# Kernel optimization log

Measured on AMD Instinct MI355X. Metric: run time of the kernel, lower is better.

## Reference

```python
import jax, jax.numpy as jnp
import numpy as np

DIM = 1024
D_STATE = 64
D_CONV = 4
EXPAND = 2
HEADDIM = 64
D_INNER = EXPAND * DIM                      # 2048
NHEADS = D_INNER // HEADDIM                 # 32
D_CONV_DIM = D_INNER + 2 * D_STATE          # 2176 (ngroups=1)
D_IN_PROJ = 2 * D_INNER + 2 * D_STATE + NHEADS  # 4256


def setup_inputs() -> dict:
    key = jax.random.key(0)
    ks = jax.random.split(key, 9)
    B, L = 4, 2048
    x = jax.random.normal(ks[0], (B, L, DIM), dtype=jnp.float32)
    in_proj_w = jax.random.normal(ks[1], (D_IN_PROJ, DIM), dtype=jnp.float32) * 0.02
    conv_w = jax.random.normal(ks[2], (D_CONV_DIM, D_CONV), dtype=jnp.float32) * 0.2
    conv_b = jax.random.normal(ks[3], (D_CONV_DIM,), dtype=jnp.float32) * 0.02
    # dt bias from inverse-softplus of dt ~ U(1e-3, 0.1) (mamba2 init)
    dt = jnp.exp(jax.random.uniform(ks[4], (NHEADS,)) * (np.log(0.1) - np.log(1e-3)) + np.log(1e-3))
    dt_bias = (dt + jnp.log(-jnp.expm1(-dt))).astype(jnp.float32)
    A_log = jnp.log(jax.random.uniform(ks[5], (NHEADS,), minval=1.0, maxval=16.0)).astype(jnp.float32)
    D = jnp.ones((NHEADS,), dtype=jnp.float32)
    norm_w = jnp.ones((D_INNER,), dtype=jnp.float32)
    out_proj_w = jax.random.normal(ks[6], (DIM, D_INNER), dtype=jnp.float32) * 0.02
    return {"x": x, "in_proj_w": in_proj_w, "conv_w": conv_w, "conv_b": conv_b,
            "dt_bias": dt_bias, "A_log": A_log, "D": D, "norm_w": norm_w,
            "out_proj_w": out_proj_w}


def _mamba2_fwd(x, in_proj_w, conv_w, conv_b, dt_bias, A_log, D, norm_w, out_proj_w):
    B, L, _ = x.shape
    zxbcdt = jnp.einsum('bld,ed->ble', x, in_proj_w)  # (B,L,4256)
    z = zxbcdt[..., :D_INNER]
    xBC = zxbcdt[..., D_INNER:D_INNER + D_CONV_DIM]
    dt = jax.nn.softplus(zxbcdt[..., D_INNER + D_CONV_DIM:] + dt_bias)  # (B,L,H)
    # causal depthwise conv (kernel D_CONV) + silu
    xp = jnp.pad(xBC, ((0, 0), (D_CONV - 1, 0), (0, 0)))
    conv = conv_b
    for k in range(D_CONV):
        conv = conv + xp[:, k:k + L, :] * conv_w[:, k]
    xBC = jax.nn.silu(conv)
    x_ssm = xBC[..., :D_INNER].reshape(B, L, NHEADS, HEADDIM)
    Bm = xBC[..., D_INNER:D_INNER + D_STATE]          # (B,L,N) ngroups=1
    Cm = xBC[..., D_INNER + D_STATE:]                 # (B,L,N)
    A = -jnp.exp(A_log)                               # (H,)

    def step(h, inp):
        xt, Bt, Ct, dtt = inp                         # (B,H,P),(B,N),(B,N),(B,H)
        dA = jnp.exp(dtt * A)                         # (B,H)
        h = h * dA[:, :, None, None] + (dtt[:, :, None] * xt)[..., None] * Bt[:, None, None, :]
        y = jnp.einsum('bhpn,bn->bhp', h, Ct)
        return h, y

    h0 = jnp.zeros((B, NHEADS, HEADDIM, D_STATE), dtype=x.dtype)
    xs = (jnp.swapaxes(x_ssm, 0, 1), jnp.swapaxes(Bm, 0, 1),
          jnp.swapaxes(Cm, 0, 1), jnp.swapaxes(dt, 0, 1))
    _, ys = jax.lax.scan(step, h0, xs)                # (L,B,H,P)
    y = jnp.swapaxes(ys, 0, 1) + x_ssm * D[None, None, :, None]
    y = y.reshape(B, L, D_INNER)
    # gated RMSNorm (norm_before_gate=False): norm(y * silu(z))
    g = y * jax.nn.silu(z)
    g = g * jax.lax.rsqrt(jnp.mean(g * g, axis=-1, keepdims=True) + 1e-5) * norm_w
    return jnp.einsum('ble,de->bld', g, out_proj_w)


def reference(x, in_proj_w, conv_w, conv_b, dt_bias, A_log, D, norm_w, out_proj_w):
    return _mamba2_fwd(x, in_proj_w, conv_w, conv_b, dt_bias, A_log, D, norm_w, out_proj_w)
```

## Files before the change

### kernel.cpp

```cpp
#include <hip/hip_runtime.h>
#include <stdint.h>

typedef unsigned short ushort_t;
typedef __attribute__((ext_vector_type(4))) float f32x4;
typedef __attribute__((ext_vector_type(8))) short short8;
typedef __attribute__((ext_vector_type(4))) unsigned short us4;

#define L_SEQ   2048
#define NROWS   8192
#define KDIM    1024
#define DINNER  2048
#define NHEADS  32
#define DSTATE  64
#define DCONVD  2176
#define NPROJ   4256
#define NPROJP  4352
#define LDZX    4352
#define NCHUNK  32

__device__ __forceinline__ float bf2f(ushort_t u) {
    union { uint32_t i; float f; } v; v.i = ((uint32_t)u) << 16; return v.f;
}
__device__ __forceinline__ ushort_t f2bf(float f) {
    uint32_t x = __float_as_uint(f);
    x += 0x7FFFu + ((x >> 16) & 1u);
    return (ushort_t)(x >> 16);
}
__device__ __forceinline__ int swzi(int row, int col) {
    return row * 64 + (col ^ ((row & 7) << 3));
}

__global__ __launch_bounds__(256) void cast_bf16_kernel(const float* __restrict__ in,
                                                        ushort_t* __restrict__ out, int n4) {
    int i = blockIdx.x * 256 + threadIdx.x;
    if (i >= n4) return;
    float4 v = ((const float4*)in)[i];
    ushort4 o;
    o.x = f2bf(v.x); o.y = f2bf(v.y); o.z = f2bf(v.z); o.w = f2bf(v.w);
    ((ushort4*)out)[i] = o;
}

__global__ __launch_bounds__(256) void cast_pad_w_kernel(const float* __restrict__ w,
                                                         ushort_t* __restrict__ out) {
    int i = blockIdx.x * 256 + threadIdx.x;
    int idx = i * 4;
    int row = idx >> 10;
    ushort4 o;
    if (row < NPROJ) {
        float4 v = ((const float4*)w)[i];
        o.x = f2bf(v.x); o.y = f2bf(v.y); o.z = f2bf(v.z); o.w = f2bf(v.w);
    } else {
        o.x = 0; o.y = 0; o.z = 0; o.w = 0;
    }
    ((ushort4*)out)[i] = o;
}

__device__ __forceinline__ void async16(const void* g, void* l) {
    __builtin_amdgcn_global_load_lds((const __attribute__((address_space(1))) void*)g,
                                     (__attribute__((address_space(3))) void*)l, 16, 0, 0);
}

template<bool OUT_BF16>
__global__ __launch_bounds__(256) void gemm_bt_kernel(const ushort_t* __restrict__ A,
                                                      const ushort_t* __restrict__ B,
                                                      void* __restrict__ Cp,
                                                      const int K, const int ldc) {
    __shared__ ushort_t As[4096];
    __shared__ ushort_t Bs[4096];
    const int tid  = threadIdx.x;
    const int wave = tid >> 6;
    const int lane = tid & 63;
    const int llo  = lane & 15;
    const int lhi  = lane >> 4;
    const int m0 = blockIdx.y * 128;
    const int n0 = blockIdx.x * 128;
    const int wr = wave >> 1, wc = wave & 1;

    f32x4 acc[4][4];
    const f32x4 zero = {0.f, 0.f, 0.f, 0.f};
#pragma unroll
    for (int i = 0; i < 4; ++i)
#pragma unroll
        for (int j = 0; j < 4; ++j) acc[i][j] = zero;

    const int srow = tid >> 2;
    const int skq  = tid & 3;
    const ushort_t* gA = A + (size_t)(m0 + srow) * K + skq * 8;
    const ushort_t* gB = B + (size_t)(n0 + srow) * K + skq * 8;
    ushort_t* lA0 = As + wave * 512;
    ushort_t* lA1 = As + 2048 + wave * 512;
    ushort_t* lB0 = Bs + wave * 512;
    ushort_t* lB1 = Bs + 2048 + wave * 512;
    const size_t rstep = (size_t)64 * K;

    const ushort_t* pa = As + (wr * 64 + llo) * 32 + lhi * 8;
    const ushort_t* pb = Bs + (wc * 64 + llo) * 32 + lhi * 8;

    for (int k0 = 0; k0 < K; k0 += 32) {
        __syncthreads();
        async16(gA + k0, lA0);
        async16(gA + rstep + k0, lA1);
        async16(gB + k0, lB0);
        async16(gB + rstep + k0, lB1);
        __syncthreads();
        short8 af[4], bfr[4];
#pragma unroll
        for (int i = 0; i < 4; ++i) af[i]  = *(const short8*)(pa + i * 512);
#pragma unroll
        for (int j = 0; j < 4; ++j) bfr[j] = *(const short8*)(pb + j * 512);
#pragma unroll
        for (int i = 0; i < 4; ++i)
#pragma unroll
            for (int j = 0; j < 4; ++j)
                acc[i][j] = __builtin_amdgcn_mfma_f32_16x16x32_bf16(af[i], bfr[j], acc[i][j], 0, 0, 0);
    }

#pragma unroll
    for (int i = 0; i < 4; ++i)
#pragma unroll
        for (int j = 0; j < 4; ++j) {
            const int col = n0 + wc * 64 + j * 16 + llo;
            const int rowb = m0 + wr * 64 + i * 16 + lhi * 4;
#pragma unroll
            for (int r = 0; r < 4; ++r) {
                if (OUT_BF16) {
                    ((ushort_t*)Cp)[(size_t)(rowb + r) * ldc + col] = f2bf(acc[i][j][r]);
                } else {
                    ((float*)Cp)[(size_t)(rowb + r) * ldc + col] = acc[i][j][r];
                }
            }
        }
}

__global__ __launch_bounds__(256) void conv_silu_kernel(const ushort_t* __restrict__ zx,
                                                        const float* __restrict__ conv_w,
                                                        const float* __restrict__ conv_b,
                                                        ushort_t* __restrict__ convout) {
    const int c = blockIdx.x * 256 + threadIdx.x;
    const int row = blockIdx.y;
    if (c >= DCONVD) return;
    const int l = row & (L_SEQ - 1);
    float acc = conv_b[c];
#pragma unroll
    for (int k = 0; k < 4; ++k) {
        int ll = l - 3 + k;
        if (ll >= 0)
            acc += bf2f(zx[(size_t)(row - 3 + k) * LDZX + DINNER + c]) * conv_w[c * 4 + k];
    }
    float s = acc / (1.f + expf(-acc));
    convout[(size_t)row * DCONVD + c] = f2bf(s);
}

__global__ __launch_bounds__(256) void dt_kernel(const ushort_t* __restrict__ zx,
                                                 const float* __restrict__ dt_bias,
                                                 float* __restrict__ dtb) {
    int idx = blockIdx.x * 256 + threadIdx.x;
    int row = idx >> 5;
    int h = idx & 31;
    float v = bf2f(zx[(size_t)row * LDZX + NPROJ - NHEADS + h]) + dt_bias[h];
    dtb[idx] = (v > 20.f) ? v : log1pf(expf(v));
}

__global__ __launch_bounds__(256) void chunk_intra_kernel(
    const ushort_t* __restrict__ cvb, const float* __restrict__ dtb,
    const float* __restrict__ A_log, const float* __restrict__ Dvec,
    ushort_t* __restrict__ ybuf, ushort_t* __restrict__ Gbuf,
    float* __restrict__ expPb)
{
    const int c = blockIdx.x, h = blockIdx.y, b = blockIdx.z;
    const int tid = threadIdx.x;
    const int wv = tid >> 6, lane = tid & 63;
    const int lr = lane & 15, lk = lane >> 4;

    __shared__ __align__(16) ushort_t Cs[4096];
    __shared__ __align__(16) ushort_t Bs[4096];
    __shared__ __align__(16) ushort_t Xt[4096];
    __shared__ __align__(16) ushort_t Ss[4096];
    __shared__ __align__(16) ushort_t Bw[4096];
    __shared__ float sP[64], sdt[64], sWf[64];

    const int t4 = tid >> 2, qq = tid & 3;
    const size_t rowg0 = (size_t)b * L_SEQ + c * 64;
    const ushort_t* rowp = cvb + (rowg0 + t4) * DCONVD;

    short8 rb0 = *(const short8*)(rowp + DINNER + qq * 16);
    short8 rb1 = *(const short8*)(rowp + DINNER + qq * 16 + 8);
    short8 rc0 = *(const short8*)(rowp + DINNER + DSTATE + qq * 16);
    short8 rc1 = *(const short8*)(rowp + DINNER + DSTATE + qq * 16 + 8);
    short8 rx0 = *(const short8*)(rowp + h * 64 + qq * 16);
    short8 rx1 = *(const short8*)(rowp + h * 64 + qq * 16 + 8);

    *(short8*)&Cs[swzi(t4, qq * 16)]     = rc0;
    *(short8*)&Cs[swzi(t4, qq * 16 + 8)] = rc1;
    *(short8*)&Bs[swzi(t4, qq * 16)]     = rb0;
    *(short8*)&Bs[swzi(t4, qq * 16 + 8)] = rb1;
#pragma unroll
    for (int k = 0; k < 8; ++k) {
        Xt[swzi(qq * 16 + k, t4)]     = (ushort_t)rx0[k];
        Xt[swzi(qq * 16 + 8 + k, t4)] = (ushort_t)rx1[k];
    }
    if (tid < 64) {
        float dt = dtb[(rowg0 + tid) * NHEADS + h];
        float A = -__expf(A_log[h]);
        float P = dt * A;
#pragma unroll
        for (int off = 1; off < 64; off <<= 1) {
            float o = __shfl_up(P, off);
            if (tid >= off) P += o;
        }
        sP[tid] = P;
        sdt[tid] = dt;
        float P63 = __shfl(P, 63);
        sWf[tid] = __expf(P63 - P) * dt;
        expPb[(size_t)(b * NHEADS + h) * L_SEQ + c * 64 + tid] = __expf(P);
    }
    __syncthreads();

    {
        const float w = sWf[t4];
#pragma unroll
        for (int k = 0; k < 8; ++k) {
            Bw[swzi(qq * 16 + k, t4)]     = f2bf(bf2f((ushort_t)rb0[k]) * w);
            Bw[swzi(qq * 16 + 8 + k, t4)] = f2bf(bf2f((ushort_t)rb1[k]) * w);
        }
    }

    const float Dh = Dvec[h];
    {
        short8 a0 = *(const short8*)&Cs[swzi(wv * 16 + lr, lk * 8)];
        short8 a1 = *(const short8*)&Cs[swzi(wv * 16 + lr, 32 + lk * 8)];
        f32x4 acc[4];
        const f32x4 zero = {0.f, 0.f, 0.f, 0.f};
#pragma unroll
        for (int nj = 0; nj < 4; ++nj) {
            short8 b0 = *(const short8*)&Bs[swzi(nj * 16 + lr, lk * 8)];
            short8 b1 = *(const short8*)&Bs[swzi(nj * 16 + lr, 32 + lk * 8)];
            acc[nj] = __builtin_amdgcn_mfma_f32_16x16x32_bf16(a0, b0, zero, 0, 0, 0);
            acc[nj] = __builtin_amdgcn_mfma_f32_16x16x32_bf16(a1, b1, acc[nj], 0, 0, 0);
        }
#pragma unroll
        for (int r = 0; r < 4; ++r) {
            const int i = wv * 16 + lk * 4 + r;
            const float Pi = sP[i];
#pragma unroll
            for (int nj = 0; nj < 4; ++nj) {
                const int j = nj * 16 + lr;
                float s = 0.f;
                if (j <= i) s = acc[nj][r] * __expf(Pi - sP[j]) * sdt[j];
                if (j == i) s += Dh;
                Ss[swzi(i, j)] = f2bf(s);
            }
        }
    }
    __syncthreads();

    {
        short8 a0 = *(const short8*)&Ss[swzi(wv * 16 + lr, lk * 8)];
        short8 a1 = *(const short8*)&Ss[swzi(wv * 16 + lr, 32 + lk * 8)];
        const f32x4 zero = {0.f, 0.f, 0.f, 0.f};
#pragma unroll
        for (int np = 0; np < 4; ++np) {
            short8 b0 = *(const short8*)&Xt[swzi(np * 16 + lr, lk * 8)];
            short8 b1 = *(const short8*)&Xt[swzi(np * 16 + lr, 32 + lk * 8)];
            f32x4 acc = __builtin_amdgcn_mfma_f32_16x16x32_bf16(a0, b0, zero, 0, 0, 0);
            acc = __builtin_amdgcn_mfma_f32_16x16x32_bf16(a1, b1, acc, 0, 0, 0);
#pragma unroll
            for (int r = 0; r < 4; ++r) {
                const int i = wv * 16 + lk * 4 + r;
                const int p = np * 16 + lr;
                ybuf[(rowg0 + i) * DINNER + (size_t)h * 64 + p] = f2bf(acc[r]);
            }
        }
    }

    {
        short8 a0 = *(const short8*)&Xt[swzi(wv * 16 + lr, lk * 8)];
        short8 a1 = *(const short8*)&Xt[swzi(wv * 16 + lr, 32 + lk * 8)];
        const f32x4 zero = {0.f, 0.f, 0.f, 0.f};
        const size_t gbase = ((size_t)((b * NHEADS + h) * NCHUNK + c)) << 12;
#pragma unroll
        for (int nt = 0; nt < 4; ++nt) {
            short8 b0 = *(const short8*)&Bw[swzi(nt * 16 + lr, lk * 8)];
            short8 b1 = *(const short8*)&Bw[swzi(nt * 16 + lr, 32 + lk * 8)];
            f32x4 acc = __builtin_amdgcn_mfma_f32_16x16x32_bf16(a0, b0, zero, 0, 0, 0);
            acc = __builtin_amdgcn_mfma_f32_16x16x32_bf16(a1, b1, acc, 0, 0, 0);
#pragma unroll
            for (int r = 0; r < 4; ++r) {
                const int p = wv * 16 + lk * 4 + r;
                const int n = nt * 16 + lr;
                Gbuf[gbase + p * 64 + n] = f2bf(acc[r]);
            }
        }
    }
}

__global__ __launch_bounds__(256) void state_scan_kernel(
    ushort_t* __restrict__ GH, const float* __restrict__ expPb)
{
    const int half = blockIdx.x, h = blockIdx.y, b = blockIdx.z;
    const int bh = b * NHEADS + h;
    const int e0 = half * 2048 + threadIdx.x * 8;
    ushort_t* base = GH + ((size_t)bh << 17);
    const float* ep = expPb + (size_t)bh * L_SEQ;

    float hr[8];
#pragma unroll
    for (int k = 0; k < 8; ++k) hr[k] = 0.f;

    short8 g = *(const short8*)(base + e0);
    float Ec = ep[63];
    for (int c = 0; c < NCHUNK; ++c) {
        short8 gn = g; float En = 0.f;
        if (c + 1 < NCHUNK) {
            gn = *(const short8*)(base + ((size_t)(c + 1) << 12) + e0);
            En = ep[(c + 1) * 64 + 63];
        }
        short8 o;
#pragma unroll
        for (int k = 0; k < 8; ++k) o[k] = (short)f2bf(hr[k]);
        *(short8*)(base + ((size_t)c << 12) + e0) = o;
#pragma unroll
        for (int k = 0; k < 8; ++k) hr[k] = hr[k] * Ec + bf2f((ushort_t)g[k]);
        g = gn; Ec = En;
    }
}

__global__ __launch_bounds__(256) void y_inter_kernel(
    const ushort_t* __restrict__ cvb, const float* __restrict__ expPb,
    const ushort_t* __restrict__ hst, ushort_t* __restrict__ ybuf)
{
    const int c = blockIdx.x + 1, h = blockIdx.y, b = blockIdx.z;
    const int tid = threadIdx.x;
    const int wv = tid >> 6, lane = tid & 63;
    const int lr = lane & 15, lk = lane >> 4;
    const int bh = b * NHEADS + h;

    __shared__ __align__(16) ushort_t Cs[4096];
    __shared__ __align__(16) ushort_t Hp[4096];
    __shared__ float sEp[64];

    const int t4 = tid >> 2, qq = tid & 3;
    const size_t rowg0 = (size_t)b * L_SEQ + c * 64;
    {
        const ushort_t* rp = cvb + (rowg0 + t4) * DCONVD + DINNER + DSTATE + qq * 16;
        *(short8*)&Cs[swzi(t4, qq * 16)]     = *(const short8*)rp;
        *(short8*)&Cs[swzi(t4, qq * 16 + 8)] = *(const short8*)(rp + 8);
        const ushort_t* hr = hst + (((size_t)(bh * NCHUNK + c)) << 12) + t4 * 64 + qq * 16;
        *(short8*)&Hp[swzi(t4, qq * 16)]     = *(const short8*)hr;
        *(short8*)&Hp[swzi(t4, qq * 16 + 8)] = *(const short8*)(hr + 8);
    }
    if (tid < 64) sEp[tid] = expPb[(size_t)bh * L_SEQ + c * 64 + tid];
    __syncthreads();

    short8 a0 = *(const short8*)&Cs[swzi(wv * 16 + lr, lk * 8)];
    short8 a1 = *(const short8*)&Cs[swzi(wv * 16 + lr, 32 + lk * 8)];
    const f32x4 zero = {0.f, 0.f, 0.f, 0.f};
#pragma unroll
    for (int np = 0; np < 4; ++np) {
        short8 b0 = *(const short8*)&Hp[swzi(np * 16 + lr, lk * 8)];
        short8 b1 = *(const short8*)&Hp[swzi(np * 16 + lr, 32 + lk * 8)];
        f32x4 acc = __builtin_amdgcn_mfma_f32_16x16x32_bf16(a0, b0, zero, 0, 0, 0);
        acc = __builtin_amdgcn_mfma_f32_16x16x32_bf16(a1, b1, acc, 0, 0, 0);
#pragma unroll
        for (int r = 0; r < 4; ++r) {
            const int t = wv * 16 + lk * 4 + r;
            const int p = np * 16 + lr;
            ushort_t* yp = &ybuf[(rowg0 + t) * DINNER + (size_t)h * 64 + p];
            *yp = f2bf(bf2f(*yp) + acc[r] * sEp[t]);
        }
    }
}

__global__ __launch_bounds__(256) void gatenorm_kernel(const ushort_t* __restrict__ ybuf,
                                                       const ushort_t* __restrict__ zx,
                                                       const float* __restrict__ norm_w,
                                                       ushort_t* __restrict__ gbuf) {
    const int row = blockIdx.x;
    const int tid = threadIdx.x;
    short8 yv = *(const short8*)(ybuf + (size_t)row * DINNER + tid * 8);
    short8 zv = *(const short8*)(zx + (size_t)row * LDZX + tid * 8);
    float g[8];
    float ss = 0.f;
#pragma unroll
    for (int i = 0; i < 8; ++i) {
        float y = bf2f((ushort_t)yv[i]);
        float z = bf2f((ushort_t)zv[i]);
        float sz = z / (1.f + expf(-z));
        float gg = y * sz;
        g[i] = gg;
        ss += gg * gg;
    }
#pragma unroll
    for (int o = 32; o > 0; o >>= 1) ss += __shfl_xor(ss, o);
    __shared__ float wsum[4];
    if ((tid & 63) == 0) wsum[tid >> 6] = ss;
    __syncthreads();
    float tot = wsum[0] + wsum[1] + wsum[2] + wsum[3];
    float scale = rsqrtf(tot * (1.0f / (float)DINNER) + 1e-5f);
    short8 o8;
#pragma unroll
    for (int i = 0; i < 8; ++i)
        o8[i] = (short)f2bf(g[i] * scale * norm_w[tid * 8 + i]);
    *(short8*)(gbuf + (size_t)row * DINNER + tid * 8) = o8;
}

extern "C" void kernel_launch(void* const* d_in, const int* in_sizes, int n_in,
                              void* d_out, int out_size, void* d_ws, size_t ws_size,
                              hipStream_t stream) {
    const float* x          = (const float*)d_in[0];
    const float* in_proj_w  = (const float*)d_in[1];
    const float* conv_w     = (const float*)d_in[2];
    const float* conv_b     = (const float*)d_in[3];
    const float* dt_bias    = (const float*)d_in[4];
    const float* A_log      = (const float*)d_in[5];
    const float* Dvec       = (const float*)d_in[6];
    const float* norm_w     = (const float*)d_in[7];
    const float* out_proj_w = (const float*)d_in[8];
    float* out = (float*)d_out;

    char* ws = (char*)d_ws;
    size_t off = 0;
    ushort_t* owbf  = (ushort_t*)(ws + off); off += (size_t)KDIM * DINNER * 2;
    ushort_t* zx    = (ushort_t*)(ws + off); off += (size_t)NROWS * LDZX * 2;
    ushort_t* cvb   = (ushort_t*)(ws + off); off += (size_t)NROWS * DCONVD * 2;
    float*    dtb   = (float*)(ws + off);    off += (size_t)NROWS * NHEADS * 4;
    float*    expPb = (float*)(ws + off);    off += (size_t)128 * L_SEQ * 4;
    ushort_t* ybuf  = (ushort_t*)(ws + off); off += (size_t)NROWS * DINNER * 2;
    char* tail = ws + off;
    ushort_t* xbf  = (ushort_t*)tail;
    ushort_t* wbf  = (ushort_t*)(tail + (size_t)NROWS * KDIM * 2);
    ushort_t* Gbuf = (ushort_t*)tail;
    ushort_t* gbuf = (ushort_t*)tail;

    cast_bf16_kernel<<<8192, 256, 0, stream>>>(x, xbf, NROWS * KDIM / 4);
    cast_pad_w_kernel<<<4352, 256, 0, stream>>>(in_proj_w, wbf);
    cast_bf16_kernel<<<2048, 256, 0, stream>>>(out_proj_w, owbf, KDIM * DINNER / 4);

    gemm_bt_kernel<true><<<dim3(NPROJP / 128, NROWS / 128), 256, 0, stream>>>(
        xbf, wbf, zx, KDIM, LDZX);

    conv_silu_kernel<<<dim3((DCONVD + 255) / 256, NROWS), 256, 0, stream>>>(zx, conv_w, conv_b, cvb);

    dt_kernel<<<NROWS * NHEADS / 256, 256, 0, stream>>>(zx, dt_bias, dtb);

    chunk_intra_kernel<<<dim3(NCHUNK, NHEADS, 4), 256, 0, stream>>>(
        cvb, dtb, A_log, Dvec, ybuf, Gbuf, expPb);
    state_scan_kernel<<<dim3(2, NHEADS, 4), 256, 0, stream>>>(Gbuf, expPb);
    y_inter_kernel<<<dim3(NCHUNK - 1, NHEADS, 4), 256, 0, stream>>>(
        cvb, expPb, Gbuf, ybuf);

    gatenorm_kernel<<<NROWS, 256, 0, stream>>>(ybuf, zx, norm_w, gbuf);

    gemm_bt_kernel<false><<<dim3(KDIM / 128, NROWS / 128), 256, 0, stream>>>(
        gbuf, owbf, out, DINNER, KDIM);
}
```

Baseline: 345.5 us.

## Replace in_proj GEMM with 256x256-tile double-buffered MFMA kernel

Adds a dedicated in-projection GEMM that uses 256x256 output tiles, 512 threads, XOR-swizzled LDS, and double-buffered async global-to-LDS loads interleaved with MFMA quarters. It also remaps block indices so neighbouring blocks share operand tiles in cache. The aim is more data reuse per LDS load and better overlap of loads with compute than the 128x128 kernel gives. In exchange, occupancy is one block per CU and the 544-block grid is small, which can cause tail imbalance.

```diff
diff --git a/kernel.cpp b/kernel.cpp
--- a/kernel.cpp
+++ b/kernel.cpp
@@ -58,6 +58,110 @@
 __device__ __forceinline__ void async16(const void* g, void* l) {
     __builtin_amdgcn_global_load_lds((const __attribute__((address_space(1))) void*)g,
                                      (__attribute__((address_space(3))) void*)l, 16, 0, 0);
+}
+
+__global__ __launch_bounds__(512, 1) void gemm256_kernel(const ushort_t* __restrict__ A,
+                                                         const ushort_t* __restrict__ B,
+                                                         ushort_t* __restrict__ C) {
+    __shared__ ushort_t lds[2][2][2][8192];
+    const int tid = threadIdx.x;
+    const int w = tid >> 6, l = tid & 63;
+    const int lr = l & 15, lk = l >> 4;
+    const int wm = w >> 2, wn = w & 3;
+
+    const int lin = blockIdx.x;
+    const int swz = (lin & 7) * 68 + (lin >> 3);
+    const int nt = swz % 17, mt = swz / 17;
+    const int m0 = mt * 256, n0 = nt * 256;
+
+    const int row0 = tid >> 3,          c0 = (tid & 7) ^ (row0 & 7);
+    const int row1 = (512 + tid) >> 3,  c1 = ((512 + tid) & 7) ^ (row1 & 7);
+
+    f32x4 acc[8][4];
+    const f32x4 zero = {0.f, 0.f, 0.f, 0.f};
+#pragma unroll
+    for (int i = 0; i < 8; ++i)
+#pragma unroll
+        for (int j = 0; j < 4; ++j) acc[i][j] = zero;
+
+#define STAGE256(d_, mat_, h_, ktn_) do {                                              \
+        const ushort_t* gb_ = ((mat_) == 0 ? A + (size_t)(m0 + (h_) * 128) * KDIM      \
+                                           : B + (size_t)(n0 + (h_) * 128) * KDIM)     \
+                              + (ktn_) * 64;                                           \
+        async16(gb_ + (size_t)row0 * KDIM + c0 * 8, &lds[d_][mat_][h_][w * 512]);      \
+        async16(gb_ + (size_t)row1 * KDIM + c1 * 8, &lds[d_][mat_][h_][4096 + w * 512]);\
+    } while (0)
+
+    STAGE256(0, 0, 0, 0);
+    STAGE256(0, 1, 0, 0);
+    STAGE256(0, 0, 1, 0);
+    STAGE256(0, 1, 1, 0);
+
+    const int NKT = KDIM / 64;
+    for (int kt = 0; kt < NKT; ++kt) {
+        const int d = kt & 1;
+        const ushort_t* Ah = &lds[d][0][wm][0];
+        const ushort_t* Bh = &lds[d][1][wn >> 1][0];
+        const int bcol0 = (wn & 1) * 64;
+#pragma unroll
+        for (int q = 0; q < 4; ++q) {
+            const int qm = q >> 1, qn = q & 1;
+            if (kt + 1 < NKT) {
+                STAGE256(d ^ 1, (q & 1), (q >> 1), kt + 1);
+            }
+            if (q == 0) {
+                if (kt + 1 < NKT) asm volatile("s_waitcnt vmcnt(2)" ::: "memory");
+                else              asm volatile("s_waitcnt vmcnt(0)" ::: "memory");
+            }
+            __builtin_amdgcn_s_barrier();
+            asm volatile("" ::: "memory");
+            short8 af[4][2], bfv[2][2];
+#pragma unroll
+            for (int fr = 0; fr < 4; ++fr) {
+                const int ar = qm * 64 + fr * 16 + lr;
+                const int x7 = ar & 7;
+#pragma unroll
+                for (int ks = 0; ks < 2; ++ks) {
+                    const int k16 = ks * 4 + lk;
+                    af[fr][ks] = *(const short8*)&Ah[ar * 64 + ((k16 ^ x7) << 3)];
+                }
+            }
+#pragma unroll
+            for (int fc = 0; fc < 2; ++fc) {
+                const int br = bcol0 + qn * 32 + fc * 16 + lr;
+                const int x7 = br & 7;
+#pragma unroll
+                for (int ks = 0; ks < 2; ++ks) {
+                    const int k16 = ks * 4 + lk;
+                    bfv[fc][ks] = *(const short8*)&Bh[br * 64 + ((k16 ^ x7) << 3)];
+                }
+            }
+            __builtin_amdgcn_s_setprio(1);
+#pragma unroll
+            for (int ks = 0; ks < 2; ++ks)
+#pragma unroll
+                for (int fr = 0; fr < 4; ++fr)
+#pragma unroll
+                    for (int fc = 0; fc < 2; ++fc)
+                        acc[qm * 4 + fr][qn * 2 + fc] = __builtin_amdgcn_mfma_f32_16x16x32_bf16(
+                            af[fr][ks], bfv[fc][ks], acc[qm * 4 + fr][qn * 2 + fc], 0, 0, 0);
+            __builtin_amdgcn_s_setprio(0);
+            asm volatile("" ::: "memory");
+            __builtin_amdgcn_s_barrier();
+        }
+    }
+
+#pragma unroll
+    for (int fr2 = 0; fr2 < 8; ++fr2)
+#pragma unroll
+        for (int fc2 = 0; fc2 < 4; ++fc2) {
+            const int col = n0 + wn * 64 + fc2 * 16 + lr;
+            const int rowb = m0 + wm * 128 + fr2 * 16 + lk * 4;
+#pragma unroll
+            for (int r = 0; r < 4; ++r)
+                C[(size_t)(rowb + r) * LDZX + col] = f2bf(acc[fr2][fc2][r]);
+        }
+#undef STAGE256
 }
 
 template<bool OUT_BF16>
@@ -436,8 +540,7 @@
     cast_pad_w_kernel<<<4352, 256, 0, stream>>>(in_proj_w, wbf);
     cast_bf16_kernel<<<2048, 256, 0, stream>>>(out_proj_w, owbf, KDIM * DINNER / 4);
 
-    gemm_bt_kernel<true><<<dim3(NPROJP / 128, NROWS / 128), 256, 0, stream>>>(
-        xbf, wbf, zx, KDIM, LDZX);
+    gemm256_kernel<<<544, 512, 0, stream>>>(xbf, wbf, zx);
 
     conv_silu_kernel<<<dim3((DCONVD + 255) / 256, NROWS), 256, 0, stream>>>(zx, conv_w, conv_b, cvb);
 
```

Result: no change. 340.9 us (-1.3%).

## Replace GEMMs with 256-row double-buffered swizzled-LDS tiles; vectorize conv

Applied to the files above, without the earlier changes.

Both projection GEMMs move to a new 512-thread kernel with 256xBN tiles, a K-step of 64, double-buffered async global-to-LDS loads, XOR-swizzled LDS layout to avoid bank conflicts, grid swizzling for L2 locality, and setprio around the MFMA block. This aims to raise data reuse and overlap loads with compute, compared with the old 128x128 single-buffered loop that synchronised twice per step. The conv+silu kernel now handles 8 channels per thread with vector loads and stores. The larger tiles mean fewer blocks (544 and 256), which risks lower occupancy and poor wave balance on the GPU.

```diff
diff --git a/kernel.cpp b/kernel.cpp
--- a/kernel.cpp
+++ b/kernel.cpp
@@ -60,74 +60,109 @@
                                      (__attribute__((address_space(3))) void*)l, 16, 0, 0);
 }
 
-template<bool OUT_BF16>
-__global__ __launch_bounds__(256) void gemm_bt_kernel(const ushort_t* __restrict__ A,
-                                                      const ushort_t* __restrict__ B,
-                                                      void* __restrict__ Cp,
-                                                      const int K, const int ldc) {
-    __shared__ ushort_t As[4096];
-    __shared__ ushort_t Bs[4096];
-    const int tid  = threadIdx.x;
-    const int wave = tid >> 6;
-    const int lane = tid & 63;
-    const int llo  = lane & 15;
-    const int lhi  = lane >> 4;
-    const int m0 = blockIdx.y * 128;
-    const int n0 = blockIdx.x * 128;
-    const int wr = wave >> 1, wc = wave & 1;
-
-    f32x4 acc[4][4];
+template<int BN, bool OUT_BF16>
+__global__ __launch_bounds__(512, 1) void gemm256_kernel(const ushort_t* __restrict__ Ap,
+                                                         const ushort_t* __restrict__ Bp,
+                                                         void* __restrict__ Cp,
+                                                         const int K, const int ldc,
+                                                         const int ntn) {
+    constexpr int NBH = BN / 128;
+    constexpr int FC  = BN / 64;
+    __shared__ ushort_t ldsA[2][2][8192];
+    __shared__ ushort_t ldsB[2][NBH][8192];
+
+    const int tid = threadIdx.x;
+    const int w = tid >> 6, l = tid & 63;
+    const int lr = l & 15, lk = l >> 4;
+    const int wm = w >> 2, wn = w & 3;
+
+    const int lin = blockIdx.x;
+    const int cpx = gridDim.x >> 3;
+    const int swz = (lin & 7) * cpx + (lin >> 3);
+    const int nt = swz % ntn, mt = swz / ntn;
+    const int m0 = mt * 256, n0 = nt * BN;
+
+    const int row0 = tid >> 3,          c0 = (tid & 7) ^ (row0 & 7);
+    const int row1 = (512 + tid) >> 3,  c1 = ((512 + tid) & 7) ^ (row1 & 7);
+
+    const int bcol = wn * (BN / 4);
+    const int bh = bcol >> 7, bw0 = bcol & 127;
+
+    f32x4 acc[8][FC];
     const f32x4 zero = {0.f, 0.f, 0.f, 0.f};
 #pragma unroll
-    for (int i = 0; i < 4; ++i)
-#pragma unroll
-        for (int j = 0; j < 4; ++j) acc[i][j] = zero;
-
-    const int srow = tid >> 2;
-    const int skq  = tid & 3;
-    const ushort_t* gA = A + (size_t)(m0 + srow) * K + skq * 8;
-    const ushort_t* gB = B + (size_t)(n0 + srow) * K + skq * 8;
-    ushort_t* lA0 = As + wave * 512;
-    ushort_t* lA1 = As + 2048 + wave * 512;
-    ushort_t* lB0 = Bs + wave * 512;
-    ushort_t* lB1 = Bs + 2048 + wave * 512;
-    const size_t rstep = (size_t)64 * K;
-
-    const ushort_t* pa = As + (wr * 64 + llo) * 32 + lhi * 8;
-    const ushort_t* pb = Bs + (wc * 64 + llo) * 32 + lhi * 8;
-
-    for (int k0 = 0; k0 < K; k0 += 32) {
-        __syncthreads();
-        async16(gA + k0, lA0);
-        async16(gA + rstep + k0, lA1);
-        async16(gB + k0, lB0);
-        async16(gB + rstep + k0, lB1);
-        __syncthreads();
-        short8 af[4], bfr[4];
-#pragma unroll
-        for (int i = 0; i < 4; ++i) af[i]  = *(const short8*)(pa + i * 512);
-#pragma unroll
-        for (int j = 0; j < 4; ++j) bfr[j] = *(const short8*)(pb + j * 512);
-#pragma unroll
-        for (int i = 0; i < 4; ++i)
-#pragma unroll
-            for (int j = 0; j < 4; ++j)
-                acc[i][j] = __builtin_amdgcn_mfma_f32_16x16x32_bf16(af[i], bfr[j], acc[i][j], 0, 0, 0);
-    }
-
-#pragma unroll
-    for (int i = 0; i < 4; ++i)
-#pragma unroll
-        for (int j = 0; j < 4; ++j) {
-            const int col = n0 + wc * 64 + j * 16 + llo;
-            const int rowb = m0 + wr * 64 + i * 16 + lhi * 4;
+    for (int i = 0; i < 8; ++i)
+#pragma unroll
+        for (int j = 0; j < FC; ++j) acc[i][j] = zero;
+
+    auto stage = [&](int d_, int isB, int h_, int ktn) {
+        const ushort_t* gb = (isB ? Bp + (size_t)(n0 + h_ * 128) * K
+                                  : Ap + (size_t)(m0 + h_ * 128) * K) + (size_t)ktn * 64;
+        ushort_t* lb = isB ? &ldsB[d_][h_][0] : &ldsA[d_][h_][0];
+        async16(gb + (size_t)row0 * K + c0 * 8, lb + w * 512);
+        async16(gb + (size_t)row1 * K + c1 * 8, lb + 4096 + w * 512);
+    };
+
+#define COMPUTE_KS(ks_) do {                                                          \
+        short8 af[8], bfv[FC];                                                        \
+        _Pragma("unroll")                                                             \
+        for (int fr = 0; fr < 8; ++fr) {                                              \
+            const int ar = fr * 16 + lr;                                              \
+            af[fr] = *(const short8*)&Ah[ar * 64 + ((((ks_) * 4 + lk) ^ (ar & 7)) << 3)]; \
+        }                                                                             \
+        _Pragma("unroll")                                                             \
+        for (int fc = 0; fc < FC; ++fc) {                                             \
+            const int br = bw0 + fc * 16 + lr;                                        \
+            bfv[fc] = *(const short8*)&Bh[br * 64 + ((((ks_) * 4 + lk) ^ (br & 7)) << 3)]; \
+        }                                                                             \
+        __builtin_amdgcn_s_setprio(1);                                                \
+        _Pragma("unroll")                                                             \
+        for (int fr = 0; fr < 8; ++fr)                                                \
+            _Pragma("unroll")                                                         \
+            for (int fc = 0; fc < FC; ++fc)                                           \
+                acc[fr][fc] = __builtin_amdgcn_mfma_f32_16x16x32_bf16(                \
+                    af[fr], bfv[fc], acc[fr][fc], 0, 0, 0);                           \
+        __builtin_amdgcn_s_setprio(0);                                                \
+    } while (0)
+
+    stage(0, 0, 0, 0); stage(0, 1, 0, 0);
+    stage(0, 0, 1, 0);
+    if (NBH == 2) stage(0, 1, 1, 0);
+
+    const int NKT = K >> 6;
+    for (int kt = 0; kt < NKT; ++kt) {
+        const int d = kt & 1;
+        const bool more = (kt + 1 < NKT);
+        const ushort_t* Ah = &ldsA[d][wm][0];
+        const ushort_t* Bh = &ldsB[d][bh][0];
+
+        if (more) { stage(d ^ 1, 0, 0, kt + 1); stage(d ^ 1, 1, 0, kt + 1); }
+        if (more) asm volatile("s_waitcnt vmcnt(4)" ::: "memory");
+        else      asm volatile("s_waitcnt vmcnt(0)" ::: "memory");
+        __builtin_amdgcn_s_barrier();
+
+        COMPUTE_KS(0);
+
+        if (more) { stage(d ^ 1, 0, 1, kt + 1); if (NBH == 2) stage(d ^ 1, 1, 1, kt + 1); }
+
+        COMPUTE_KS(1);
+
+        __builtin_amdgcn_s_barrier();
+    }
+#undef COMPUTE_KS
+
+#pragma unroll
+    for (int fr2 = 0; fr2 < 8; ++fr2)
+#pragma unroll
+        for (int fc2 = 0; fc2 < FC; ++fc2) {
+            const int col = n0 + bcol + fc2 * 16 + lr;
+            const int rowb = m0 + wm * 128 + fr2 * 16 + lk * 4;
 #pragma unroll
             for (int r = 0; r < 4; ++r) {
-                if (OUT_BF16) {
-                    ((ushort_t*)Cp)[(size_t)(rowb + r) * ldc + col] = f2bf(acc[i][j][r]);
-                } else {
-                    ((float*)Cp)[(size_t)(rowb + r) * ldc + col] = acc[i][j][r];
-                }
+                if (OUT_BF16)
+                    ((ushort_t*)Cp)[(size_t)(rowb + r) * ldc + col] = f2bf(acc[fr2][fc2][r]);
+                else
+                    ((float*)Cp)[(size_t)(rowb + r) * ldc + col] = acc[fr2][fc2][r];
             }
         }
 }
@@ -136,19 +171,43 @@
                                                         const float* __restrict__ conv_w,
                                                         const float* __restrict__ conv_b,
                                                         ushort_t* __restrict__ convout) {
-    const int c = blockIdx.x * 256 + threadIdx.x;
-    const int row = blockIdx.y;
-    if (c >= DCONVD) return;
+    const int idx = blockIdx.x * 256 + threadIdx.x;
+    const int row = idx / 272;
+    const int c = (idx - row * 272) * 8;
     const int l = row & (L_SEQ - 1);
-    float acc = conv_b[c];
+    float acc[8];
+    {
+        const float4* bp = (const float4*)(conv_b + c);
+        float4 b0 = bp[0], b1 = bp[1];
+        acc[0] = b0.x; acc[1] = b0.y; acc[2] = b0.z; acc[3] = b0.w;
+        acc[4] = b1.x; acc[5] = b1.y; acc[6] = b1.z; acc[7] = b1.w;
+    }
+    float wv[8][4];
+    {
+        const float4* wp = (const float4*)(conv_w + c * 4);
+#pragma unroll
+        for (int i = 0; i < 8; ++i) {
+            float4 t = wp[i];
+            wv[i][0] = t.x; wv[i][1] = t.y; wv[i][2] = t.z; wv[i][3] = t.w;
+        }
+    }
 #pragma unroll
     for (int k = 0; k < 4; ++k) {
-        int ll = l - 3 + k;
-        if (ll >= 0)
-            acc += bf2f(zx[(size_t)(row - 3 + k) * LDZX + DINNER + c]) * conv_w[c * 4 + k];
-    }
-    float s = acc / (1.f + expf(-acc));
-    convout[(size_t)row * DCONVD + c] = f2bf(s);
+        const int ll = l - 3 + k;
+        if (ll >= 0) {
+            short8 v = *(const short8*)(zx + (size_t)(row - 3 + k) * LDZX + DINNER + c);
+#pragma unroll
+            for (int i = 0; i < 8; ++i)
+                acc[i] += bf2f((ushort_t)v[i]) * wv[i][k];
+        }
+    }
+    short8 o;
+#pragma unroll
+    for (int i = 0; i < 8; ++i) {
+        float s = acc[i] / (1.f + expf(-acc[i]));
+        o[i] = (short)f2bf(s);
+    }
+    *(short8*)(convout + (size_t)row * DCONVD + c) = o;
 }
 
 __global__ __launch_bounds__(256) void dt_kernel(const ushort_t* __restrict__ zx,
@@ -436,10 +495,9 @@
     cast_pad_w_kernel<<<4352, 256, 0, stream>>>(in_proj_w, wbf);
     cast_bf16_kernel<<<2048, 256, 0, stream>>>(out_proj_w, owbf, KDIM * DINNER / 4);
 
-    gemm_bt_kernel<true><<<dim3(NPROJP / 128, NROWS / 128), 256, 0, stream>>>(
-        xbf, wbf, zx, KDIM, LDZX);
-
-    conv_silu_kernel<<<dim3((DCONVD + 255) / 256, NROWS), 256, 0, stream>>>(zx, conv_w, conv_b, cvb);
+    gemm256_kernel<256, true><<<544, 512, 0, stream>>>(xbf, wbf, zx, KDIM, LDZX, 17);
+
+    conv_silu_kernel<<<NROWS * 272 / 256, 256, 0, stream>>>(zx, conv_w, conv_b, cvb);
 
     dt_kernel<<<NROWS * NHEADS / 256, 256, 0, stream>>>(zx, dt_bias, dtb);
 
@@ -451,6 +509,5 @@
 
     gatenorm_kernel<<<NROWS, 256, 0, stream>>>(ybuf, zx, norm_w, gbuf);
 
-    gemm_bt_kernel<false><<<dim3(KDIM / 128, NROWS / 128), 256, 0, stream>>>(
-        gbuf, owbf, out, DINNER, KDIM);
-}
+    gemm256_kernel<128, false><<<256, 512, 0, stream>>>(gbuf, owbf, out, DINNER, KDIM, 8);
+}
```

Measured after the change: 329.2 us. 4.7% less time.
